# Kernel optimization log

Measured on AMD Instinct MI355X. Metric: run time of the kernel, lower is better.

The kernel has to match this reference:

```python
import jax, jax.numpy as jnp
import numpy as np

H = 16      # num_heads
D = 64      # nhid (per-head dim)
SL, BS = 1024, 64
DM = 1024   # keys_dim == query_dim == values_dim

def setup_inputs() -> dict:
    key = jax.random.key(0)
    k1, k2, k3, k4, k5 = jax.random.split(key, 5)
    return {
        "query":  jax.random.normal(k1, (BS, DM), dtype=jnp.float32),
        "keys":   jax.random.normal(k2, (SL, BS, DM), dtype=jnp.float32),
        "values": jax.random.normal(k3, (SL, BS, DM), dtype=jnp.float32),
        "Wq":     jax.random.normal(k4, (H * D, DM), dtype=jnp.float32) * 0.02,
        "Wk":     jax.random.normal(k5, (H * D, DM), dtype=jnp.float32) * 0.02,
    }

def reference(query, keys, values, Wq, Wk):
    bs = query.shape[0]
    sl = keys.shape[0]
    scale = jnp.asarray(np.sqrt(D), dtype=query.dtype)
    # projections (note: original module applies keys_linear to values -- a bug we replicate)
    qp = (query @ Wq.T).reshape(bs, H, D)                 # [bs, H, D]
    kp = (keys @ Wk.T).reshape(sl, bs, H, D)              # [sl, bs, H, D]
    vp = (values @ Wk.T).reshape(sl, bs, H, D)            # [sl, bs, H, D]
    # per-head scaled dot-product scores, softmax over the sequence axis (dim 0)
    scores = jnp.einsum('bhd,sbhd->sbh', qp, kp) / scale  # [sl, bs, H]
    attn = jax.nn.softmax(scores, axis=0)
    out = jnp.einsum('sbh,sbhd->bhd', attn, vp)           # [bs, H, D]
    return out.reshape(bs, H * D)
```

## Files before the change

kernel.cpp:

```cpp
#include <hip/hip_runtime.h>
#include <cstddef>
#include <cstdint>

#define NH 16
#define HD 64
#define SLEN 1024
#define NB 64
#define DMODEL 1024

#define DOT4_ACC(acc, k, q) \
  acc = fmaf((k).x, (q).x, fmaf((k).y, (q).y, fmaf((k).z, (q).z, fmaf((k).w, (q).w, (acc)))))

#define FMA4_BCAST(accv, qv, w0_, w1_, w2_, w3_) do { \
  (accv).x = fmaf((qv).x, (w0_).x, fmaf((qv).y, (w1_).x, fmaf((qv).z, (w2_).x, fmaf((qv).w, (w3_).x, (accv).x)))); \
  (accv).y = fmaf((qv).x, (w0_).y, fmaf((qv).y, (w1_).y, fmaf((qv).z, (w2_).y, fmaf((qv).w, (w3_).y, (accv).y)))); \
  (accv).z = fmaf((qv).x, (w0_).z, fmaf((qv).y, (w1_).z, fmaf((qv).z, (w2_).z, fmaf((qv).w, (w3_).z, (accv).z)))); \
  (accv).w = fmaf((qv).x, (w0_).w, fmaf((qv).y, (w1_).w, fmaf((qv).z, (w2_).w, fmaf((qv).w, (w3_).w, (accv).w)))); \
} while (0)

__device__ __forceinline__ float wred_sum(float v) {
#pragma unroll
  for (int off = 32; off; off >>= 1) v += __shfl_xor(v, off, 64);
  return v;
}

__global__ __launch_bounds__(256) void k0_qp(const float* __restrict__ query,
                                             const float* __restrict__ Wq,
                                             float* __restrict__ qp) {
  const int tid = threadIdx.x;
  const int w = tid >> 6, l = tid & 63;
  const int j = blockIdx.x * 4 + w;
  const float4* wr = reinterpret_cast<const float4*>(Wq + (size_t)j * DMODEL) + l * 4;
  const float4 w0 = wr[0], w1 = wr[1], w2 = wr[2], w3 = wr[3];
  for (int b = 0; b < NB; ++b) {
    const float4* qr = reinterpret_cast<const float4*>(query + (size_t)b * DMODEL) + l * 4;
    float4 q0 = qr[0], q1 = qr[1], q2 = qr[2], q3 = qr[3];
    float s = 0.f;
    DOT4_ACC(s, w0, q0); DOT4_ACC(s, w1, q1); DOT4_ACC(s, w2, q2); DOT4_ACC(s, w3, q3);
    s = wred_sum(s);
    if (l == 0) qp[(size_t)b * DMODEL + j] = s;
  }
}

__global__ __launch_bounds__(256) void k1_qt(const float* __restrict__ qp,
                                             const float* __restrict__ Wk,
                                             float* __restrict__ qt) {
  __shared__ __align__(16) float qpl[8][HD];
  const int h = blockIdx.x & 15;
  const int b0 = (blockIdx.x >> 4) * 8;
  const int tid = threadIdx.x;
  for (int f = tid; f < 8 * HD; f += 256) {
    int bi = f >> 6, d = f & 63;
    qpl[bi][d] = qp[(size_t)(b0 + bi) * DMODEL + h * HD + d];
  }
  __syncthreads();
  const int m4 = tid * 4;
  float4 acc[8];
#pragma unroll
  for (int i = 0; i < 8; ++i) acc[i] = make_float4(0.f, 0.f, 0.f, 0.f);
  const float* wbase = Wk + (size_t)(h * HD) * DMODEL + m4;
  for (int d = 0; d < HD; d += 4) {
    float4 wk0 = *reinterpret_cast<const float4*>(wbase + (size_t)(d + 0) * DMODEL);
    float4 wk1 = *reinterpret_cast<const float4*>(wbase + (size_t)(d + 1) * DMODEL);
    float4 wk2 = *reinterpret_cast<const float4*>(wbase + (size_t)(d + 2) * DMODEL);
    float4 wk3 = *reinterpret_cast<const float4*>(wbase + (size_t)(d + 3) * DMODEL);
#pragma unroll
    for (int bi = 0; bi < 8; ++bi) {
      float4 q = *reinterpret_cast<const float4*>(&qpl[bi][d]);
      FMA4_BCAST(acc[bi], q, wk0, wk1, wk2, wk3);
    }
  }
#pragma unroll
  for (int bi = 0; bi < 8; ++bi)
    *reinterpret_cast<float4*>(qt + ((size_t)(b0 + bi) * NH + h) * DMODEL + m4) = acc[bi];
}

__global__ __launch_bounds__(128) void k2_scores(const float* __restrict__ keys,
                                                 const float* __restrict__ qt,
                                                 float* __restrict__ sc) {
  __shared__ __align__(16) float ql[NH][512];
  const int b  = blockIdx.x & 63;
  const int st = blockIdx.x >> 6;
  const int tid = threadIdx.x, w = tid >> 6, l = tid & 63;
  const int hg = l & 3;
  const int sg = l >> 2;
  const int s_a = st * 64 + w * 32 + sg;
  const int s_b = s_a + 16;
  const float* ka = keys + ((size_t)s_a * NB + b) * DMODEL + hg * 4;
  const float* kb = keys + ((size_t)s_b * NB + b) * DMODEL + hg * 4;
  float acc0[NH], acc1[NH];
#pragma unroll
  for (int hh = 0; hh < NH; ++hh) { acc0[hh] = 0.f; acc1[hh] = 0.f; }

  for (int ph = 0; ph < 2; ++ph) {
    __syncthreads();
    for (int f = tid; f < 2048; f += 128) {
      int hh = f >> 7, m4 = (f & 127) * 4;
      *reinterpret_cast<float4*>(&ql[hh][m4]) = *reinterpret_cast<const float4*>(
          qt + ((size_t)b * NH + hh) * DMODEL + ph * 512 + m4);
    }
    __syncthreads();
    const float* kpa = ka + ph * 512;
    const float* kpb = kb + ph * 512;
#pragma unroll 4
    for (int m = 0; m < 512; m += 16) {
      float4 k0 = *reinterpret_cast<const float4*>(kpa + m);
      float4 k1 = *reinterpret_cast<const float4*>(kpb + m);
#pragma unroll
      for (int hh = 0; hh < NH; ++hh) {
        float4 q = *reinterpret_cast<const float4*>(&ql[hh][m + hg * 4]);
        DOT4_ACC(acc0[hh], k0, q);
        DOT4_ACC(acc1[hh], k1, q);
      }
    }
  }
#pragma unroll
  for (int hh = 0; hh < NH; ++hh) {
    acc0[hh] += __shfl_xor(acc0[hh], 1, 64); acc0[hh] += __shfl_xor(acc0[hh], 2, 64);
    acc1[hh] += __shfl_xor(acc1[hh], 1, 64); acc1[hh] += __shfl_xor(acc1[hh], 2, 64);
  }
  const float scale = 0.125f;
#pragma unroll
  for (int j = 0; j < 4; ++j) {
    float r0 = hg == 0 ? acc0[j] : hg == 1 ? acc0[4 + j] : hg == 2 ? acc0[8 + j] : acc0[12 + j];
    float r1 = hg == 0 ? acc1[j] : hg == 1 ? acc1[4 + j] : hg == 2 ? acc1[8 + j] : acc1[12 + j];
    float* o = sc + ((size_t)b * NH + hg * 4 + j) * SLEN;
    o[s_a] = r0 * scale;
    o[s_b] = r1 * scale;
  }
}

__global__ __launch_bounds__(256) void k_sm(float* __restrict__ sc) {
  __shared__ float red[8];
  const int tid = threadIdx.x, w = tid >> 6, l = tid & 63;
  float* p = sc + (size_t)blockIdx.x * SLEN;
  float4 x = reinterpret_cast<const float4*>(p)[tid];
  float mx = fmaxf(fmaxf(x.x, x.y), fmaxf(x.z, x.w));
#pragma unroll
  for (int off = 32; off; off >>= 1) mx = fmaxf(mx, __shfl_xor(mx, off, 64));
  if (l == 0) red[w] = mx;
  __syncthreads();
  mx = fmaxf(fmaxf(red[0], red[1]), fmaxf(red[2], red[3]));
  float4 e;
  e.x = __expf(x.x - mx); e.y = __expf(x.y - mx);
  e.z = __expf(x.z - mx); e.w = __expf(x.w - mx);
  float sum = e.x + e.y + e.z + e.w;
  sum = wred_sum(sum);
  if (l == 0) red[4 + w] = sum;
  __syncthreads();
  sum = red[4] + red[5] + red[6] + red[7];
  const float inv = 1.f / sum;
  e.x *= inv; e.y *= inv; e.z *= inv; e.w *= inv;
  reinterpret_cast<float4*>(p)[tid] = e;
}

template <int NCH>
__global__ __launch_bounds__(256) void k3_cpart(const float* __restrict__ values,
                                                const float* __restrict__ attn,
                                                float* __restrict__ cp) {
  constexpr int SC = SLEN / NCH;
  const int b = blockIdx.x & 63;
  const int ch = blockIdx.x >> 6;
  const int s0 = ch * SC;
  const int tid = threadIdx.x;
  const int m4 = tid * 4;
  float4 acc[NH];
#pragma unroll
  for (int i = 0; i < NH; ++i) acc[i] = make_float4(0.f, 0.f, 0.f, 0.f);
  const float* vbase = values + ((size_t)s0 * NB + b) * DMODEL + m4;
  const float* abase = attn + (size_t)b * NH * SLEN + s0;
#pragma unroll 2
  for (int sl = 0; sl < SC; sl += 4) {
    const float* vp = vbase + (size_t)sl * NB * DMODEL;
    float4 v0 = *reinterpret_cast<const float4*>(vp);
    float4 v1 = *reinterpret_cast<const float4*>(vp + (size_t)1 * NB * DMODEL);
    float4 v2 = *reinterpret_cast<const float4*>(vp + (size_t)2 * NB * DMODEL);
    float4 v3 = *reinterpret_cast<const float4*>(vp + (size_t)3 * NB * DMODEL);
#pragma unroll
    for (int hh = 0; hh < NH; ++hh) {
      float4 a = *reinterpret_cast<const float4*>(abase + hh * SLEN + sl);
      FMA4_BCAST(acc[hh], a, v0, v1, v2, v3);
    }
  }
#pragma unroll
  for (int hh = 0; hh < NH; ++hh)
    *reinterpret_cast<float4*>(cp + (((size_t)ch * NB + b) * NH + hh) * DMODEL + m4) = acc[hh];
}

template <int NCH>
__global__ __launch_bounds__(256) void k4_out(const float* __restrict__ cp,
                                              const float* __restrict__ Wk,
                                              float* __restrict__ out) {
  __shared__ __align__(16) float cl[4 * DMODEL];
  const int h = blockIdx.x & 15;
  const int b0 = (blockIdx.x >> 4) * 4;
  const int tid = threadIdx.x, w = tid >> 6, l = tid & 63;
  for (int f = tid; f < 4 * DMODEL / 4; f += 256) {
    int bi = f >> 8, m4 = (f & 255) * 4;
    float4 s = make_float4(0.f, 0.f, 0.f, 0.f);
#pragma unroll
    for (int ch = 0; ch < NCH; ++ch) {
      float4 t = *reinterpret_cast<const float4*>(
          cp + (((size_t)ch * NB + b0 + bi) * NH + h) * DMODEL + m4);
      s.x += t.x; s.y += t.y; s.z += t.z; s.w += t.w;
    }
    *reinterpret_cast<float4*>(&cl[bi * DMODEL + m4]) = s;
  }
  __syncthreads();
  float4 c[4][4];
#pragma unroll
  for (int bi = 0; bi < 4; ++bi)
#pragma unroll
    for (int k = 0; k < 4; ++k)
      c[bi][k] = *reinterpret_cast<const float4*>(&cl[bi * DMODEL + l * 16 + k * 4]);
  for (int jj = 0; jj < 16; ++jj) {
    const int d = w * 16 + jj;
    const float4* wr = reinterpret_cast<const float4*>(Wk + (size_t)(h * HD + d) * DMODEL) + l * 4;
    const float4 w0 = wr[0], w1 = wr[1], w2 = wr[2], w3 = wr[3];
#pragma unroll
    for (int bi = 0; bi < 4; ++bi) {
      float s = 0.f;
      DOT4_ACC(s, w0, c[bi][0]); DOT4_ACC(s, w1, c[bi][1]);
      DOT4_ACC(s, w2, c[bi][2]); DOT4_ACC(s, w3, c[bi][3]);
      s = wred_sum(s);
      if (l == 0) out[(size_t)(b0 + bi) * (NH * HD) + h * HD + d] = s;
    }
  }
}

extern "C" void kernel_launch(void* const* d_in, const int* in_sizes, int n_in,
                              void* d_out, int out_size, void* d_ws, size_t ws_size,
                              hipStream_t stream) {
  const float* query  = (const float*)d_in[0];
  const float* keys   = (const float*)d_in[1];
  const float* values = (const float*)d_in[2];
  const float* Wq     = (const float*)d_in[3];
  const float* Wk     = (const float*)d_in[4];
  float* out = (float*)d_out;

  float* W  = (float*)d_ws;
  float* qp = W;
  float* qt = qp + (size_t)NB * DMODEL;
  float* sc = qt + (size_t)NB * NH * DMODEL;
  float* cp = sc + (size_t)NB * NH * SLEN;

  const size_t base_floats = (size_t)NB * DMODEL + 2 * (size_t)NB * NH * DMODEL;

  k0_qp<<<256, 256, 0, stream>>>(query, Wq, qp);
  k1_qt<<<128, 256, 0, stream>>>(qp, Wk, qt);
  k2_scores<<<1024, 128, 0, stream>>>(keys, qt, sc);
  k_sm<<<NB * NH, 256, 0, stream>>>(sc);

  const size_t chunk_floats = (size_t)NB * NH * DMODEL;
  if (ws_size >= (base_floats + 16 * chunk_floats) * sizeof(float)) {
    k3_cpart<16><<<16 * NB, 256, 0, stream>>>(values, sc, cp);
    k4_out<16><<<NH * (NB / 4), 256, 0, stream>>>(cp, Wk, out);
  } else if (ws_size >= (base_floats + 8 * chunk_floats) * sizeof(float)) {
    k3_cpart<8><<<8 * NB, 256, 0, stream>>>(values, sc, cp);
    k4_out<8><<<NH * (NB / 4), 256, 0, stream>>>(cp, Wk, out);
  } else if (ws_size >= (base_floats + 4 * chunk_floats) * sizeof(float)) {
    k3_cpart<4><<<4 * NB, 256, 0, stream>>>(values, sc, cp);
    k4_out<4><<<NH * (NB / 4), 256, 0, stream>>>(cp, Wk, out);
  } else {
    k3_cpart<2><<<2 * NB, 256, 0, stream>>>(values, sc, cp);
    k4_out<2><<<NH * (NB / 4), 256, 0, stream>>>(cp, Wk, out);
  }
}
```

Measured before the change: 255.3 us.

## Split score reduction across model-dim halves and stage attention weights in LDS

The scores kernel now splits the 1024-wide reduction into two halves handled by separate blocks, each loading its q slice into LDS once and computing four sequence rows per thread instead of two. The two partial score planes are written separately and summed inside the softmax kernel. This removes the second LDS reload phase and the extra barriers, and it doubles the rows that reuse each LDS q read. The value-weighting kernel now stages its attention chunk in shared memory instead of reading it repeatedly from global memory. In exchange there is extra workspace, an extra partial-score read in softmax, and more accumulator registers in the scores kernel.

After: 255.0 us. No clear change (-0.1%).

```diff
diff --git a/kernel.cpp b/kernel.cpp
--- a/kernel.cpp
+++ b/kernel.cpp
@@ -77,64 +77,75 @@
 
 __global__ __launch_bounds__(128) void k2_scores(const float* __restrict__ keys,
                                                  const float* __restrict__ qt,
-                                                 float* __restrict__ sc) {
+                                                 float* __restrict__ scp) {
   __shared__ __align__(16) float ql[NH][512];
   const int b  = blockIdx.x & 63;
-  const int st = blockIdx.x >> 6;
+  const int st = (blockIdx.x >> 6) & 7;
+  const int mh = blockIdx.x >> 9;
   const int tid = threadIdx.x, w = tid >> 6, l = tid & 63;
   const int hg = l & 3;
   const int sg = l >> 2;
-  const int s_a = st * 64 + w * 32 + sg;
-  const int s_b = s_a + 16;
-  const float* ka = keys + ((size_t)s_a * NB + b) * DMODEL + hg * 4;
-  const float* kb = keys + ((size_t)s_b * NB + b) * DMODEL + hg * 4;
-  float acc0[NH], acc1[NH];
-#pragma unroll
-  for (int hh = 0; hh < NH; ++hh) { acc0[hh] = 0.f; acc1[hh] = 0.f; }
-
-  for (int ph = 0; ph < 2; ++ph) {
-    __syncthreads();
-    for (int f = tid; f < 2048; f += 128) {
-      int hh = f >> 7, m4 = (f & 127) * 4;
-      *reinterpret_cast<float4*>(&ql[hh][m4]) = *reinterpret_cast<const float4*>(
-          qt + ((size_t)b * NH + hh) * DMODEL + ph * 512 + m4);
-    }
-    __syncthreads();
-    const float* kpa = ka + ph * 512;
-    const float* kpb = kb + ph * 512;
+  for (int f = tid; f < 2048; f += 128) {
+    int hh = f >> 7, m4 = (f & 127) * 4;
+    *reinterpret_cast<float4*>(&ql[hh][m4]) = *reinterpret_cast<const float4*>(
+        qt + ((size_t)b * NH + hh) * DMODEL + mh * 512 + m4);
+  }
+  __syncthreads();
+  const int s_base = st * 128 + w * 64 + sg;
+  const float* kp0 = keys + ((size_t)(s_base +  0) * NB + b) * DMODEL + mh * 512 + hg * 4;
+  const float* kp1 = keys + ((size_t)(s_base + 16) * NB + b) * DMODEL + mh * 512 + hg * 4;
+  const float* kp2 = keys + ((size_t)(s_base + 32) * NB + b) * DMODEL + mh * 512 + hg * 4;
+  const float* kp3 = keys + ((size_t)(s_base + 48) * NB + b) * DMODEL + mh * 512 + hg * 4;
+  float acc[4][NH];
+#pragma unroll
+  for (int si = 0; si < 4; ++si)
+#pragma unroll
+    for (int hh = 0; hh < NH; ++hh) acc[si][hh] = 0.f;
 #pragma unroll 4
-    for (int m = 0; m < 512; m += 16) {
-      float4 k0 = *reinterpret_cast<const float4*>(kpa + m);
-      float4 k1 = *reinterpret_cast<const float4*>(kpb + m);
-#pragma unroll
-      for (int hh = 0; hh < NH; ++hh) {
-        float4 q = *reinterpret_cast<const float4*>(&ql[hh][m + hg * 4]);
-        DOT4_ACC(acc0[hh], k0, q);
-        DOT4_ACC(acc1[hh], k1, q);
-      }
-    }
-  }
-#pragma unroll
-  for (int hh = 0; hh < NH; ++hh) {
-    acc0[hh] += __shfl_xor(acc0[hh], 1, 64); acc0[hh] += __shfl_xor(acc0[hh], 2, 64);
-    acc1[hh] += __shfl_xor(acc1[hh], 1, 64); acc1[hh] += __shfl_xor(acc1[hh], 2, 64);
-  }
+  for (int m = 0; m < 512; m += 16) {
+    float4 k0 = *reinterpret_cast<const float4*>(kp0 + m);
+    float4 k1 = *reinterpret_cast<const float4*>(kp1 + m);
+    float4 k2 = *reinterpret_cast<const float4*>(kp2 + m);
+    float4 k3 = *reinterpret_cast<const float4*>(kp3 + m);
+#pragma unroll
+    for (int hh = 0; hh < NH; ++hh) {
+      float4 q = *reinterpret_cast<const float4*>(&ql[hh][m + hg * 4]);
+      DOT4_ACC(acc[0][hh], k0, q);
+      DOT4_ACC(acc[1][hh], k1, q);
+      DOT4_ACC(acc[2][hh], k2, q);
+      DOT4_ACC(acc[3][hh], k3, q);
+    }
+  }
+#pragma unroll
+  for (int si = 0; si < 4; ++si)
+#pragma unroll
+    for (int hh = 0; hh < NH; ++hh) {
+      acc[si][hh] += __shfl_xor(acc[si][hh], 1, 64);
+      acc[si][hh] += __shfl_xor(acc[si][hh], 2, 64);
+    }
   const float scale = 0.125f;
+  float* plane = scp + (size_t)mh * NB * NH * SLEN;
 #pragma unroll
   for (int j = 0; j < 4; ++j) {
-    float r0 = hg == 0 ? acc0[j] : hg == 1 ? acc0[4 + j] : hg == 2 ? acc0[8 + j] : acc0[12 + j];
-    float r1 = hg == 0 ? acc1[j] : hg == 1 ? acc1[4 + j] : hg == 2 ? acc1[8 + j] : acc1[12 + j];
-    float* o = sc + ((size_t)b * NH + hg * 4 + j) * SLEN;
-    o[s_a] = r0 * scale;
-    o[s_b] = r1 * scale;
-  }
-}
-
-__global__ __launch_bounds__(256) void k_sm(float* __restrict__ sc) {
+    float* o = plane + ((size_t)b * NH + hg * 4 + j) * SLEN + s_base;
+#pragma unroll
+    for (int si = 0; si < 4; ++si) {
+      float r = hg == 0 ? acc[si][j] : hg == 1 ? acc[si][4 + j]
+              : hg == 2 ? acc[si][8 + j] : acc[si][12 + j];
+      o[si * 16] = r * scale;
+    }
+  }
+}
+
+__global__ __launch_bounds__(256) void k_sm(float* __restrict__ sc0,
+                                            const float* __restrict__ sc1) {
   __shared__ float red[8];
   const int tid = threadIdx.x, w = tid >> 6, l = tid & 63;
-  float* p = sc + (size_t)blockIdx.x * SLEN;
-  float4 x = reinterpret_cast<const float4*>(p)[tid];
+  float* p0 = sc0 + (size_t)blockIdx.x * SLEN;
+  const float* p1 = sc1 + (size_t)blockIdx.x * SLEN;
+  float4 xa = reinterpret_cast<const float4*>(p0)[tid];
+  float4 xb = reinterpret_cast<const float4*>(p1)[tid];
+  float4 x = make_float4(xa.x + xb.x, xa.y + xb.y, xa.z + xb.z, xa.w + xb.w);
   float mx = fmaxf(fmaxf(x.x, x.y), fmaxf(x.z, x.w));
 #pragma unroll
   for (int off = 32; off; off >>= 1) mx = fmaxf(mx, __shfl_xor(mx, off, 64));
@@ -151,7 +162,7 @@
   sum = red[4] + red[5] + red[6] + red[7];
   const float inv = 1.f / sum;
   e.x *= inv; e.y *= inv; e.z *= inv; e.w *= inv;
-  reinterpret_cast<float4*>(p)[tid] = e;
+  reinterpret_cast<float4*>(p0)[tid] = e;
 }
 
 template <int NCH>
@@ -159,16 +170,22 @@
                                                 const float* __restrict__ attn,
                                                 float* __restrict__ cp) {
   constexpr int SC = SLEN / NCH;
+  __shared__ __align__(16) float al[NH * SC];
   const int b = blockIdx.x & 63;
   const int ch = blockIdx.x >> 6;
   const int s0 = ch * SC;
   const int tid = threadIdx.x;
+  for (int f = tid; f < NH * SC / 4; f += 256) {
+    int hh = f / (SC / 4), c4 = f % (SC / 4);
+    *reinterpret_cast<float4*>(&al[hh * SC + c4 * 4]) =
+        *reinterpret_cast<const float4*>(attn + ((size_t)b * NH + hh) * SLEN + s0 + c4 * 4);
+  }
+  __syncthreads();
   const int m4 = tid * 4;
   float4 acc[NH];
 #pragma unroll
   for (int i = 0; i < NH; ++i) acc[i] = make_float4(0.f, 0.f, 0.f, 0.f);
   const float* vbase = values + ((size_t)s0 * NB + b) * DMODEL + m4;
-  const float* abase = attn + (size_t)b * NH * SLEN + s0;
 #pragma unroll 2
   for (int sl = 0; sl < SC; sl += 4) {
     const float* vp = vbase + (size_t)sl * NB * DMODEL;
@@ -178,7 +195,7 @@
     float4 v3 = *reinterpret_cast<const float4*>(vp + (size_t)3 * NB * DMODEL);
 #pragma unroll
     for (int hh = 0; hh < NH; ++hh) {
-      float4 a = *reinterpret_cast<const float4*>(abase + hh * SLEN + sl);
+      float4 a = *reinterpret_cast<const float4*>(&al[hh * SC + sl]);
       FMA4_BCAST(acc[hh], a, v0, v1, v2, v3);
     }
   }
@@ -238,31 +255,33 @@
   const float* Wk     = (const float*)d_in[4];
   float* out = (float*)d_out;
 
-  float* W  = (float*)d_ws;
-  float* qp = W;
-  float* qt = qp + (size_t)NB * DMODEL;
-  float* sc = qt + (size_t)NB * NH * DMODEL;
-  float* cp = sc + (size_t)NB * NH * SLEN;
-
-  const size_t base_floats = (size_t)NB * DMODEL + 2 * (size_t)NB * NH * DMODEL;
+  float* W   = (float*)d_ws;
+  float* qp  = W;
+  float* qt  = qp + (size_t)NB * DMODEL;
+  float* sc0 = qt + (size_t)NB * NH * DMODEL;
+  float* sc1 = sc0 + (size_t)NB * NH * SLEN;
+  float* cp  = sc1 + (size_t)NB * NH * SLEN;
+
+  const size_t base_floats = (size_t)NB * DMODEL + (size_t)NB * NH * DMODEL
+                           + 2 * (size_t)NB * NH * SLEN;
 
   k0_qp<<<256, 256, 0, stream>>>(query, Wq, qp);
   k1_qt<<<128, 256, 0, stream>>>(qp, Wk, qt);
-  k2_scores<<<1024, 128, 0, stream>>>(keys, qt, sc);
-  k_sm<<<NB * NH, 256, 0, stream>>>(sc);
+  k2_scores<<<1024, 128, 0, stream>>>(keys, qt, sc0);
+  k_sm<<<NB * NH, 256, 0, stream>>>(sc0, sc1);
 
   const size_t chunk_floats = (size_t)NB * NH * DMODEL;
   if (ws_size >= (base_floats + 16 * chunk_floats) * sizeof(float)) {
-    k3_cpart<16><<<16 * NB, 256, 0, stream>>>(values, sc, cp);
+    k3_cpart<16><<<16 * NB, 256, 0, stream>>>(values, sc0, cp);
     k4_out<16><<<NH * (NB / 4), 256, 0, stream>>>(cp, Wk, out);
   } else if (ws_size >= (base_floats + 8 * chunk_floats) * sizeof(float)) {
-    k3_cpart<8><<<8 * NB, 256, 0, stream>>>(values, sc, cp);
+    k3_cpart<8><<<8 * NB, 256, 0, stream>>>(values, sc0, cp);
     k4_out<8><<<NH * (NB / 4), 256, 0, stream>>>(cp, Wk, out);
   } else if (ws_size >= (base_floats + 4 * chunk_floats) * sizeof(float)) {
-    k3_cpart<4><<<4 * NB, 256, 0, stream>>>(values, sc, cp);
+    k3_cpart<4><<<4 * NB, 256, 0, stream>>>(values, sc0, cp);
     k4_out<4><<<NH * (NB / 4), 256, 0, stream>>>(cp, Wk, out);
   } else {
-    k3_cpart<2><<<2 * NB, 256, 0, stream>>>(values, sc, cp);
+    k3_cpart<2><<<2 * NB, 256, 0, stream>>>(values, sc0, cp);
     k4_out<2><<<NH * (NB / 4), 256, 0, stream>>>(cp, Wk, out);
   }
 }
```
